# Kernel optimization log

Hardware: AMD Instinct MI355X
Metric: run time of the kernel (lower is better)

The kernel has to match this reference:

```python
import jax, jax.numpy as jnp
import numpy as np

B, N, H = 2, 1024, 768
MAX_W = 30
WIDTH_D = 20
SPAN_DIM = 3 * H + WIDTH_D  # 2324
K = int(N * 0.4)  # 409 (eval mode: // (1+0) )


def _enumerate_spans(n, max_w):
    # Replicates: enumerate_spans then sorted(spans[::-1], key=start)
    # -> start ascending, end DESCENDING within each start.
    spans = []
    for s in range(n):
        for e in range(min(s + max_w - 1, n - 1), s - 1, -1):
            spans.append((s, e))
    return np.asarray(spans, dtype=np.int32)  # [num_spans, 2]


def setup_inputs() -> dict:
    key = jax.random.key(0)
    ks = jax.random.split(key, 8)
    spans = jnp.asarray(_enumerate_spans(N, MAX_W))  # [30285, 2]
    return {
        "segment_embeddings": jax.random.normal(ks[0], (B, N, H), jnp.float32),
        "segment_mask": jnp.ones((B, N), jnp.int32),
        "candidate_spans": spans,
        "width_emb": jax.random.normal(ks[1], (MAX_W, WIDTH_D), jnp.float32) * 0.02,
        "W1": jax.random.normal(ks[2], (SPAN_DIM, H), jnp.float32) * 0.02,
        "b1": jax.random.normal(ks[3], (H,), jnp.float32) * 0.02,
        "w_s": jax.random.normal(ks[4], (H,), jnp.float32) * 0.02,
        "b_s": jax.random.normal(ks[5], (1,), jnp.float32) * 0.02,
        "k": K,
    }


def reference(segment_embeddings, segment_mask, candidate_spans, width_emb, W1, b1, w_s, b_s, k):
    starts = candidate_spans[:, 0]  # [S]
    ends = candidate_spans[:, 1]    # [S]
    # Endpoint span extractor: x, y, x*y + width embedding (width = end-start)
    x = segment_embeddings[:, starts, :]          # [B,S,H]
    y = segment_embeddings[:, ends, :]            # [B,S,H]
    wemb = width_emb[ends - starts]               # [S,WIDTH_D]
    bsz = segment_embeddings.shape[0]
    span_feat = jnp.concatenate(
        [x, y, x * y, jnp.broadcast_to(wemb[None], (bsz,) + wemb.shape)], axis=-1
    )  # [B,S,3H+WD]
    # MLP (dropout is identity in eval) + GELU (torch default: exact erf)
    h = jax.nn.gelu(jnp.einsum("bsd,dh->bsh", span_feat, W1) + b1, approximate=False)
    scores = jnp.einsum("bsh,h->bs", h, w_s) + b_s[0]  # [B,S]
    # Mask spans whose end index exceeds valid length
    lengths = segment_mask.sum(-1)  # [B]
    scores = scores + jnp.where(ends[None, :] >= lengths[:, None], -1e6, 0.0)
    # Top-k prune, then sort indices and gather
    _, idx = jax.lax.top_k(scores, k)          # [B,k]
    idx = jnp.sort(idx, axis=1)
    top_scores = jnp.take_along_axis(scores, idx, axis=1)            # [B,k]
    top_span_embs = jnp.take_along_axis(h, idx[:, :, None], axis=1)  # [B,k,H]
    top_spans = candidate_spans[idx]                                 # [B,k,2]
    return top_span_embs, top_scores, top_spans
```

## Files before the change

kernel.cpp:

```cpp
#include <hip/hip_runtime.h>
#include <math.h>

#define NB 2
#define NN 1024
#define HH 768
#define MAXW 30
#define KTOP 409
#define BANDCAP 4096
#define BAND_TAU 2e-2f
#define FILTCAP 6144
#define GROWS 512
#define WCAP 40

typedef __attribute__((ext_vector_type(4))) float f32x4;
typedef __attribute__((ext_vector_type(8))) __bf16 bf16x8;
typedef __attribute__((ext_vector_type(8))) unsigned short us8;

__device__ __forceinline__ float gelu_f(float z) {
  return 0.5f * z * (1.0f + erff(z * 0.70710678118654752440f));
}
__device__ __forceinline__ unsigned f2key(float f) {
  unsigned u = __float_as_uint(f);
  return (u & 0x80000000u) ? ~u : (u | 0x80000000u);
}
__device__ __forceinline__ float key2f(unsigned k) {
  unsigned u = (k & 0x80000000u) ? (k & 0x7fffffffu) : ~k;
  return __uint_as_float(u);
}
__device__ __forceinline__ unsigned short f2bf_rn(float f) {
  unsigned u = __float_as_uint(f);
  unsigned r = u + 0x7fffu + ((u >> 16) & 1u);
  return (unsigned short)(r >> 16);
}
__device__ __forceinline__ float bf2f(unsigned short h) {
  return __uint_as_float(((unsigned)h) << 16);
}
__device__ __forceinline__ void async_copy16(const void* g, void* l) {
  __builtin_amdgcn_global_load_lds(
      (const __attribute__((address_space(1))) unsigned int*)g,
      (__attribute__((address_space(3))) unsigned int*)l, 16, 0, 0);
}

__global__ void len_kernel(const int* __restrict__ mask, int* __restrict__ lengths) {
  __shared__ int red[256];
  for (int b = 0; b < NB; ++b) {
    int s = 0;
    for (int i = threadIdx.x; i < NN; i += 256) s += mask[b * NN + i];
    red[threadIdx.x] = s;
    __syncthreads();
    for (int off = 128; off > 0; off >>= 1) {
      if (threadIdx.x < off) red[threadIdx.x] += red[threadIdx.x + off];
      __syncthreads();
    }
    if (threadIdx.x == 0) lengths[b] = red[0];
    __syncthreads();
  }
}

__global__ void r_kernel(const float* __restrict__ wemb, const float* __restrict__ W1,
                         const float* __restrict__ b1, float* __restrict__ R) {
  int w = blockIdx.x;
  for (int h = threadIdx.x; h < HH; h += 256) {
    float acc = b1[h];
    for (int j = 0; j < 20; ++j)
      acc = fmaf(wemb[w * 20 + j], W1[(size_t)(3 * HH + j) * HH + h], acc);
    R[w * HH + h] = acc;
  }
}

__global__ __launch_bounds__(256) void prep_bt_kernel(const float* __restrict__ W1,
                                                      unsigned short* __restrict__ Bt,
                                                      unsigned short* __restrict__ Btlo) {
  const int ki = blockIdx.x;
  const int hby = blockIdx.y;
  const float* W1c = W1 + (size_t)(2 * HH) * HH;
  const int t = threadIdx.x;
#pragma unroll
  for (int half = 0; half < 2; ++half) {
    const int c = t + half * 256;
    const int col = c >> 2, kg = c & 3;
    us8 hv, lv;
#pragma unroll
    for (int j = 0; j < 8; ++j) {
      const int k = ki * 32 + kg * 8 + j;
      float v = W1c[(size_t)k * HH + hby * 128 + col];
      unsigned short h = f2bf_rn(v);
      hv[j] = h;
      lv[j] = f2bf_rn(v - bf2f(h));
    }
    const size_t bo = ((size_t)(hby * 24 + ki) * 512 + c) * 8;
    *(us8*)(Bt + bo) = hv;
    *(us8*)(Btlo + bo) = lv;
  }
}

__global__ __launch_bounds__(256) void prep_emb_hl_kernel(
    const float* __restrict__ emb, unsigned short* __restrict__ Ahi,
    unsigned short* __restrict__ Alo) {
  const int tile = blockIdx.x;
  const int ki = blockIdx.y;
  const int t = threadIdx.x;
#pragma unroll
  for (int half = 0; half < 2; ++half) {
    const int c = t + half * 256;
    const int row = c >> 2, kgs = c & 3;
    const int kg = kgs ^ ((row >> 1) & 3);
    const float* xr = emb + (size_t)(tile * 128 + row) * HH;
    const int k0 = ki * 32 + kg * 8;
    float4 x0 = *(const float4*)(xr + k0);
    float4 x1 = *(const float4*)(xr + k0 + 4);
    const float xv[8] = {x0.x, x0.y, x0.z, x0.w, x1.x, x1.y, x1.z, x1.w};
    us8 hv, lv;
#pragma unroll
    for (int j = 0; j < 8; ++j) {
      unsigned short h = f2bf_rn(xv[j]);
      hv[j] = h;
      lv[j] = f2bf_rn(xv[j] - bf2f(h));
    }
    const size_t base = (((size_t)tile * 24 + ki) * 512 + c) * 8;
    *(us8*)(Ahi + base) = hv;
    *(us8*)(Alo + base) = lv;
  }
}

__global__ __launch_bounds__(256) void prep_w1ab_kernel(
    const float* __restrict__ W1, unsigned short* __restrict__ Bhi,
    unsigned short* __restrict__ Blo) {
  const int ki = blockIdx.x;
  const int hby = blockIdx.y;
  const int t = threadIdx.x;
#pragma unroll
  for (int half = 0; half < 2; ++half) {
    const int c = t + half * 256;
    const int col = c >> 2, kg = c & 3;
    const int gc = hby * 128 + col;
    const float* base = W1 + (gc < 768 ? (size_t)0 : (size_t)HH * HH);
    const int n = (gc < 768) ? gc : gc - 768;
    us8 hv, lv;
#pragma unroll
    for (int j = 0; j < 8; ++j) {
      const int k = ki * 32 + kg * 8 + j;
      float v = base[(size_t)k * HH + n];
      unsigned short h = f2bf_rn(v);
      hv[j] = h;
      lv[j] = f2bf_rn(v - bf2f(h));
    }
    const size_t bo = (((size_t)hby * 24 + ki) * 512 + c) * 8;
    *(us8*)(Bhi + bo) = hv;
    *(us8*)(Blo + bo) = lv;
  }
}

__global__ __launch_bounds__(256) void pq_mfma_kernel(
    const unsigned short* __restrict__ Ahi, const unsigned short* __restrict__ Alo,
    const unsigned short* __restrict__ Bhi, const unsigned short* __restrict__ Blo,
    float* __restrict__ P, float* __restrict__ Q) {
  __shared__ unsigned short AsmH[128 * 32], AsmL[128 * 32];
  const int tile = blockIdx.x;
  const int hby = blockIdx.y;
  const int tid = threadIdx.x;
  const int lane = tid & 63, w = tid >> 6;
  const int wm = w & 1, wn = w >> 1;
  const int lm = lane & 15, lq = lane >> 4;

  f32x4 acc[4][4];
#pragma unroll
  for (int i = 0; i < 4; ++i)
#pragma unroll
    for (int j = 0; j < 4; ++j) acc[i][j] = (f32x4){0.f, 0.f, 0.f, 0.f};

  const unsigned short* AbH = Ahi + (size_t)tile * 24 * 4096;
  const unsigned short* AbL = Alo + (size_t)tile * 24 * 4096;
  const unsigned short* BbH = Bhi + (size_t)hby * 24 * 4096;
  const unsigned short* BbL = Blo + (size_t)hby * 24 * 4096;
  const int a_off = (wm * 64 + lm) * 32 + (lq ^ ((lm >> 1) & 3)) * 8;
  const int b_off = (wn * 64 + lm) * 32 + lq * 8;

  for (int ki = 0; ki < 24; ++ki) {
    async_copy16(AbH + (size_t)ki * 4096 + tid * 8, AsmH + tid * 8);
    async_copy16(AbH + (size_t)ki * 4096 + (tid + 256) * 8, AsmH + (tid + 256) * 8);
    async_copy16(AbL + (size_t)ki * 4096 + tid * 8, AsmL + tid * 8);
    async_copy16(AbL + (size_t)ki * 4096 + (tid + 256) * 8, AsmL + (tid + 256) * 8);
    bf16x8 bh[4], bl[4];
#pragma unroll
    for (int ni = 0; ni < 4; ++ni) {
      bh[ni] = *reinterpret_cast<const bf16x8*>(BbH + (size_t)ki * 4096 + b_off + ni * 512);
      bl[ni] = *reinterpret_cast<const bf16x8*>(BbL + (size_t)ki * 4096 + b_off + ni * 512);
    }
    __syncthreads();
    bf16x8 ah[4], al[4];
#pragma unroll
    for (int mi = 0; mi < 4; ++mi) {
      ah[mi] = *reinterpret_cast<const bf16x8*>(AsmH + a_off + mi * 512);
      al[mi] = *reinterpret_cast<const bf16x8*>(AsmL + a_off + mi * 512);
    }
#pragma unroll
    for (int ni = 0; ni < 4; ++ni)
#pragma unroll
      for (int mi = 0; mi < 4; ++mi) {
        acc[mi][ni] = __builtin_amdgcn_mfma_f32_16x16x32_bf16(ah[mi], bh[ni], acc[mi][ni], 0, 0, 0);
        acc[mi][ni] = __builtin_amdgcn_mfma_f32_16x16x32_bf16(ah[mi], bl[ni], acc[mi][ni], 0, 0, 0);
        acc[mi][ni] = __builtin_amdgcn_mfma_f32_16x16x32_bf16(al[mi], bh[ni], acc[mi][ni], 0, 0, 0);
      }
    __syncthreads();
  }

  float* Obase = (hby < 6) ? P : Q;
  const int cb = ((hby < 6) ? hby : hby - 6) * 128 + wn * 64 + lm;
  const int rowb = tile * 128 + wm * 64 + lq * 4;
#pragma unroll
  for (int mi = 0; mi < 4; ++mi)
#pragma unroll
    for (int ni = 0; ni < 4; ++ni)
#pragma unroll
      for (int r = 0; r < 4; ++r)
        Obase[(size_t)(rowb + mi * 16 + r) * HH + cb + ni * 16] = acc[mi][ni][r];
}

__global__ __launch_bounds__(512, 4) void score_mfma7_kernel(
    const float* __restrict__ emb, const int* __restrict__ spans,
    const unsigned short* __restrict__ Bt, const float* __restrict__ w_s,
    const float* __restrict__ P, const float* __restrict__ Q, const float* __restrict__ R,
    float* __restrict__ spart, int S) {
  __shared__ unsigned short Asm[128 * 32];
  __shared__ float ew[2][WCAP * 32];
  __shared__ int ssm[128], eem[128], wwm[128];
  __shared__ float sred[128 * 4];
  __shared__ int rminS, rmaxS;

  const int colblk = blockIdx.x;
  const int tile = blockIdx.y;
  const int b = blockIdx.z;
  const int tid = threadIdx.x;
  const int lane = tid & 63, w = tid >> 6;
  const int wm = w & 1, wn = w >> 1;
  const int lm = lane & 15, lq = lane >> 4;

  if (tid < 128) {
    int g = tile * 128 + tid;
    int gg = g < S ? g : S - 1;
    int s = spans[2 * gg], e = spans[2 * gg + 1];
    ssm[tid] = s; eem[tid] = e; wwm[tid] = e - s;
  }
  __syncthreads();
  if (tid == 0) {
    int rmn = ssm[0], rmx = eem[0];
    for (int i = 1; i < 128; ++i) {
      rmn = min(rmn, ssm[i]);
      rmx = max(rmx, eem[i]);
    }
    rminS = rmn; rmaxS = rmx;
  }
  __syncthreads();
  const int rmin = rminS;
  int W = rmaxS - rmin + 1;
  if (W > WCAP) W = WCAP;

  const int sr = tid >> 3, sc = (tid & 7) * 4;
  const bool stager = (tid < W * 8);
  const float* gsrc = emb + ((size_t)b * NN + rmin + sr) * HH + sc;
  const int ewoff = sr * 32 + sc;

  const int arow = tid >> 2;
  const int kgs = tid & 3;
  const int kg = kgs ^ ((arow >> 1) & 3);
  const int xo = (ssm[arow] - rmin) * 32 + kg * 8;
  const int yo = (eem[arow] - rmin) * 32 + kg * 8;
  const int aw_off = (arow * 4 + kgs) * 8;

  f32x4 acc[4][4];
#pragma unroll
  for (int i = 0; i < 4; ++i)
#pragma unroll
    for (int j = 0; j < 4; ++j) acc[i][j] = (f32x4){0.f, 0.f, 0.f, 0.f};

  const int hby = colblk * 2 + (wn >> 1);
  const unsigned short* Bb = Bt + (size_t)hby * 24 * 4096;
  const int b_off = ((wn & 1) * 64 + lm) * 32 + lq * 8;
  const int a_off = (wm * 64 + lm) * 32 + (lq ^ ((lm >> 1) & 3)) * 8;

  float4 reg = make_float4(0.f, 0.f, 0.f, 0.f);
  if (stager) {
    float4 r0 = *(const float4*)gsrc;
    *(float4*)(&ew[0][ewoff]) = r0;
    reg = *(const float4*)(gsrc + 32);
  }
  __syncthreads();

  int cur = 0;
  for (int ki = 0; ki < 24; ++ki) {
    float4 x0 = *(const float4*)(&ew[cur][xo]);
    float4 x1 = *(const float4*)(&ew[cur][xo + 4]);
    float4 y0 = *(const float4*)(&ew[cur][yo]);
    float4 y1 = *(const float4*)(&ew[cur][yo + 4]);
    us8 v;
    v[0] = f2bf_rn(x0.x * y0.x); v[1] = f2bf_rn(x0.y * y0.y);
    v[2] = f2bf_rn(x0.z * y0.z); v[3] = f2bf_rn(x0.w * y0.w);
    v[4] = f2bf_rn(x1.x * y1.x); v[5] = f2bf_rn(x1.y * y1.y);
    v[6] = f2bf_rn(x1.z * y1.z); v[7] = f2bf_rn(x1.w * y1.w);
    *(us8*)(Asm + aw_off) = v;
    if (stager && ki < 23) *(float4*)(&ew[1 - cur][ewoff]) = reg;
    __syncthreads();
    if (stager && ki + 2 < 24)
      reg = *(const float4*)(gsrc + (size_t)(ki + 2) * 32);
    bf16x8 afr[4];
#pragma unroll
    for (int mi = 0; mi < 4; ++mi)
      afr[mi] = *reinterpret_cast<const bf16x8*>(Asm + a_off + mi * 512);
#pragma unroll
    for (int ni = 0; ni < 4; ++ni) {
      bf16x8 bfr = *reinterpret_cast<const bf16x8*>(Bb + (size_t)ki * 4096 + b_off + ni * 512);
#pragma unroll
      for (int mi = 0; mi < 4; ++mi)
        acc[mi][ni] = __builtin_amdgcn_mfma_f32_16x16x32_bf16(afr[mi], bfr, acc[mi][ni], 0, 0, 0);
    }
    __syncthreads();
    cur ^= 1;
  }

  const int cbase = colblk * 256 + wn * 64 + lm;
  float wsv[4];
#pragma unroll
  for (int ni = 0; ni < 4; ++ni) wsv[ni] = w_s[cbase + ni * 16];

#pragma unroll
  for (int mi = 0; mi < 4; ++mi) {
#pragma unroll
    for (int r = 0; r < 4; ++r) {
      const int rowl = wm * 64 + mi * 16 + lq * 4 + r;
      const int s = ssm[rowl], e = eem[rowl], wd = wwm[rowl];
      const float* Pp = P + ((size_t)b * NN + s) * HH + cbase;
      const float* Qp = Q + ((size_t)b * NN + e) * HH + cbase;
      const float* Rp = R + (size_t)wd * HH + cbase;
      float psum = 0.f;
#pragma unroll
      for (int ni = 0; ni < 4; ++ni) {
        float z = acc[mi][ni][r] + Pp[ni * 16] + Qp[ni * 16] + Rp[ni * 16];
        psum = fmaf(gelu_f(z), wsv[ni], psum);
      }
      psum += __shfl_xor(psum, 1);
      psum += __shfl_xor(psum, 2);
      psum += __shfl_xor(psum, 4);
      psum += __shfl_xor(psum, 8);
      if (lm == 0) sred[rowl * 4 + wn] = psum;
    }
  }
  __syncthreads();
  if (tid < 128) {
    int g = tile * 128 + tid;
    if (g < S)
      spart[(size_t)colblk * ((size_t)NB * S) + (size_t)b * S + g] =
          sred[tid * 4] + sred[tid * 4 + 1] + sred[tid * 4 + 2] + sred[tid * 4 + 3];
  }
}

__global__ void combine_kernel(const float* __restrict__ sp, const int* __restrict__ spans,
                               const float* __restrict__ b_s, const int* __restrict__ lengths,
                               float* __restrict__ scores, int S) {
  int idx = blockIdx.x * 256 + threadIdx.x;
  if (idx >= NB * S) return;
  int b = idx / S, i = idx - b * S;
  size_t st = (size_t)NB * S;
  float v = b_s[0];
#pragma unroll
  for (int j = 0; j < 3; ++j) v += sp[j * st + idx];
  if (spans[2 * i + 1] >= lengths[b]) v += -1000000.0f;
  scores[idx] = v;
}

__global__ void zero_kernel(unsigned* __restrict__ hist, int* __restrict__ bandcount,
                            int* __restrict__ filtcount) {
  int i = blockIdx.x * 256 + threadIdx.x;
  hist[i] = 0;
  if (blockIdx.x == 0 && threadIdx.x < NB) {
    bandcount[threadIdx.x] = 0;
    filtcount[threadIdx.x] = 0;
  }
}

__global__ void hist16_kernel(const float* __restrict__ scores, unsigned* __restrict__ hist,
                              int S) {
  int idx = blockIdx.x * 256 + threadIdx.x;
  if (idx >= NB * S) return;
  int b = idx / S;
  unsigned key = f2key(scores[idx]) >> 16;
  atomicAdd(&hist[(size_t)b * 65536 + key], 1u);
}

__global__ __launch_bounds__(1024) void scan16_kernel(const unsigned* __restrict__ hist,
                                                      const int* __restrict__ kptr,
                                                      float* __restrict__ pivotf) {
  const int b = blockIdx.x;
  const unsigned* hb = hist + (size_t)b * 65536;
  const int tid = threadIdx.x;
  const unsigned k = (unsigned)kptr[0];
  __shared__ unsigned acc[1024];
  unsigned s = 0;
  for (int j = 0; j < 64; ++j) s += hb[tid * 64 + j];
  const unsigned mysum = s;
  acc[tid] = s;
  __syncthreads();
  for (int off = 1; off < 1024; off <<= 1) {
    unsigned v = (tid + off < 1024) ? acc[tid + off] : 0u;
    __syncthreads();
    acc[tid] += v;
    __syncthreads();
  }
  const unsigned above = acc[tid] - mysum;
  if (above < k && acc[tid] >= k) {
    unsigned cum = above;
    int binf = tid * 64;
    for (int j = 63; j >= 0; --j) {
      unsigned c = hb[tid * 64 + j];
      if (cum + c >= k) { binf = tid * 64 + j; break; }
      cum += c;
    }
    pivotf[b] = key2f(((unsigned)binf) << 16);
  }
}

__global__ void band_kernel(const float* __restrict__ scores, const float* __restrict__ pivotf,
                            int* __restrict__ bandcount, int* __restrict__ bandlist, int S) {
  int idx = blockIdx.x * 256 + threadIdx.x;
  if (idx >= NB * S) return;
  int b = idx / S, i = idx - b * S;
  if (fabsf(scores[idx] - pivotf[b]) <= BAND_TAU) {
    int slot = atomicAdd(&bandcount[b], 1);
    if (slot < BANDCAP) bandlist[b * BANDCAP + slot] = i;
  }
}

__global__ __launch_bounds__(256) void rescore_kernel(
    const float* __restrict__ emb, const int* __restrict__ spans,
    const float* __restrict__ W1, const float* __restrict__ w_s,
    const float* __restrict__ b_s, const int* __restrict__ lengths,
    const float* __restrict__ P, const float* __restrict__ Q, const float* __restrict__ R,
    const int* __restrict__ bandcount, const int* __restrict__ bandlist,
    float* __restrict__ scores, int S) {
  const int b = blockIdx.y;
  int cnt = bandcount[b];
  if (cnt > BANDCAP) cnt = BANDCAP;
  if ((int)blockIdx.x >= cnt) return;
  const int i = bandlist[b * BANDCAP + blockIdx.x];
  const int s = spans[2 * i], e = spans[2 * i + 1], wd = e - s;
  const int tid = threadIdx.x;
  __shared__ float prod[HH];
  __shared__ float red[256];
  for (int c = tid; c < HH; c += 256)
    prod[c] = emb[((size_t)b * NN + s) * HH + c] * emb[((size_t)b * NN + e) * HH + c];
  __syncthreads();
  const float* W1c = W1 + (size_t)(2 * HH) * HH;
  float psum = 0.f;
  for (int c0 = 0; c0 < HH; c0 += 256) {
    const int c = c0 + tid;
    float a = P[((size_t)b * NN + s) * HH + c] + Q[((size_t)b * NN + e) * HH + c] + R[(size_t)wd * HH + c];
    for (int k = 0; k < HH; ++k) a = fmaf(prod[k], W1c[(size_t)k * HH + c], a);
    psum = fmaf(gelu_f(a), w_s[c], psum);
  }
  red[tid] = psum;
  __syncthreads();
  for (int off = 128; off > 0; off >>= 1) {
    if (tid < off) red[tid] += red[tid + off];
    __syncthreads();
  }
  if (tid == 0) {
    float v = red[0] + b_s[0];
    if (e >= lengths[b]) v += -1000000.0f;
    scores[(size_t)b * S + i] = v;
  }
}

__global__ void filt_kernel(const float* __restrict__ scores, const float* __restrict__ pivotf,
                            int* __restrict__ filtcount, int* __restrict__ filtlist, int S) {
  int idx = blockIdx.x * 256 + threadIdx.x;
  if (idx >= NB * S) return;
  int b = idx / S, i = idx - b * S;
  if (scores[idx] > pivotf[b] - 0.01f) {
    int slot = atomicAdd(&filtcount[b], 1);
    if (slot < FILTCAP) filtlist[b * FILTCAP + slot] = i;
  }
}

__global__ __launch_bounds__(1024) void sel_kernel(
    const float* __restrict__ scores, const int* __restrict__ spans,
    const int* __restrict__ kptr, const int* __restrict__ filtcount,
    const int* __restrict__ filtlist,
    float* __restrict__ out_spans, int* __restrict__ sel, int S) {
  const int b = blockIdx.x;
  const int tid = threadIdx.x;
  const int k = kptr[0];
  __shared__ unsigned keys[FILTCAP];
  __shared__ int idxs[FILTCAP];
  __shared__ unsigned hist[256];
  __shared__ unsigned sh_prefix;
  __shared__ int sh_remaining;
  __shared__ int selcnt;
  __shared__ int slist[512];

  int M = filtcount[b];
  if (M > FILTCAP) M = FILTCAP;
  for (int i = tid; i < M; i += 1024) {
    int gi = filtlist[b * FILTCAP + i];
    idxs[i] = gi;
    keys[i] = f2key(scores[(size_t)b * S + gi]);
  }
  if (tid == 0) selcnt = 0;
  __syncthreads();

  unsigned prefix = 0;
  int remaining = k;
  for (int round = 0; round < 4; ++round) {
    const int shift = 24 - 8 * round;
    if (tid < 256) hist[tid] = 0;
    __syncthreads();
    for (int i = tid; i < M; i += 1024) {
      unsigned key = keys[i];
      if (round == 0 || (key >> (shift + 8)) == prefix)
        atomicAdd(&hist[(key >> shift) & 255u], 1u);
    }
    __syncthreads();
    if (tid == 0) {
      int cum = 0;
      for (int bin = 255; bin >= 0; --bin) {
        int c = (int)hist[bin];
        if (cum + c >= remaining) {
          sh_prefix = (prefix << 8) | (unsigned)bin;
          sh_remaining = remaining - cum;
          break;
        }
        cum += c;
      }
    }
    __syncthreads();
    prefix = sh_prefix;
    remaining = sh_remaining;
    __syncthreads();
  }
  const unsigned pk = prefix;
  const int m_eq = remaining;

  for (int i = tid; i < M; i += 1024) {
    unsigned key = keys[i];
    bool pick = false;
    if (key > pk) {
      pick = true;
    } else if (key == pk) {
      int r = 0;
      const int myidx = idxs[i];
      for (int j = 0; j < M; ++j)
        if (keys[j] == pk && idxs[j] < myidx) ++r;
      pick = (r < m_eq);
    }
    if (pick) {
      int p = atomicAdd(&selcnt, 1);
      if (p < 512) slist[p] = idxs[i];
    }
  }
  __syncthreads();

  for (int i = tid; i < k; i += 1024) {
    const int my = slist[i];
    int r = 0;
    for (int j = 0; j < k; ++j) r += (slist[j] < my);
    sel[b * KTOP + r] = my;
    out_spans[(b * KTOP + r) * 2 + 0] = (float)spans[2 * my];
    out_spans[(b * KTOP + r) * 2 + 1] = (float)spans[2 * my + 1];
  }
}

__global__ __launch_bounds__(256) void prep_ga_kernel(
    const float* __restrict__ emb, const int* __restrict__ spans,
    const int* __restrict__ sel, unsigned short* __restrict__ GAhi,
    unsigned short* __restrict__ GAlo) {
  const int bx = blockIdx.x;
  const int tile = bx / 24, ki = bx - tile * 24;
  const int b = blockIdx.y;
  const int t = threadIdx.x;
#pragma unroll
  for (int half = 0; half < 2; ++half) {
    const int c = t + half * 256;
    const int row = c >> 2, kgs = c & 3;
    const int kg = kgs ^ ((row >> 1) & 3);
    int j = tile * 128 + row;
    if (j >= KTOP) j = KTOP - 1;
    const int i = sel[b * KTOP + j];
    const int s = spans[2 * i], e = spans[2 * i + 1];
    const float* xr = emb + ((size_t)b * NN + s) * HH;
    const float* yr = emb + ((size_t)b * NN + e) * HH;
    const int k0 = ki * 32 + kg * 8;
    float4 x0 = *(const float4*)(xr + k0);
    float4 x1 = *(const float4*)(xr + k0 + 4);
    float4 y0 = *(const float4*)(yr + k0);
    float4 y1 = *(const float4*)(yr + k0 + 4);
    const float pv[8] = {x0.x * y0.x, x0.y * y0.y, x0.z * y0.z, x0.w * y0.w,
                         x1.x * y1.x, x1.y * y1.y, x1.z * y1.z, x1.w * y1.w};
    us8 hv, lv;
#pragma unroll
    for (int q = 0; q < 8; ++q) {
      unsigned short h = f2bf_rn(pv[q]);
      hv[q] = h;
      lv[q] = f2bf_rn(pv[q] - bf2f(h));
    }
    const size_t base = (((size_t)(b * 4 + tile) * 24 + ki) * 512 + c) * 8;
    *(us8*)(GAhi + base) = hv;
    *(us8*)(GAlo + base) = lv;
  }
}

__global__ __launch_bounds__(256) void gather_mfma_kernel(
    const int* __restrict__ spans, const int* __restrict__ sel,
    const unsigned short* __restrict__ GAhi, const unsigned short* __restrict__ GAlo,
    const unsigned short* __restrict__ Bt, const unsigned short* __restrict__ Btlo,
    const float* __restrict__ w_s,
    const float* __restrict__ P, const float* __restrict__ Q, const float* __restrict__ R,
    float* __restrict__ outh, float* __restrict__ spartg) {
  __shared__ unsigned short AsmH[128 * 32], AsmL[128 * 32];
  __shared__ int ssm[128], eem[128], wwm[128], vvm[128];
  __shared__ float sred[128 * 2];
  const int tile = blockIdx.x;
  const int hby = blockIdx.y;
  const int b = blockIdx.z;
  const int tid = threadIdx.x;
  const int lane = tid & 63, w = tid >> 6;
  const int wm = w & 1, wn = w >> 1;
  const int lm = lane & 15, lq = lane >> 4;

  if (tid < 128) {
    int j = tile * 128 + tid;
    int valid = (j < KTOP) ? 1 : 0;
    int jj = valid ? j : KTOP - 1;
    int i = sel[b * KTOP + jj];
    ssm[tid] = spans[2 * i];
    eem[tid] = spans[2 * i + 1];
    wwm[tid] = eem[tid] - ssm[tid];
    vvm[tid] = valid;
  }

  f32x4 acc[4][4];
#pragma unroll
  for (int i = 0; i < 4; ++i)
#pragma unroll
    for (int j = 0; j < 4; ++j) acc[i][j] = (f32x4){0.f, 0.f, 0.f, 0.f};

  const unsigned short* AbH = GAhi + (size_t)(b * 4 + tile) * 24 * 4096;
  const unsigned short* AbL = GAlo + (size_t)(b * 4 + tile) * 24 * 4096;
  const unsigned short* BbH = Bt + (size_t)hby * 24 * 4096;
  const unsigned short* BbL = Btlo + (size_t)hby * 24 * 4096;
  const int a_off = (wm * 64 + lm) * 32 + (lq ^ ((lm >> 1) & 3)) * 8;
  const int b_off = (wn * 64 + lm) * 32 + lq * 8;

  for (int ki = 0; ki < 24; ++ki) {
    async_copy16(AbH + (size_t)ki * 4096 + tid * 8, AsmH + tid * 8);
    async_copy16(AbH + (size_t)ki * 4096 + (tid + 256) * 8, AsmH + (tid + 256) * 8);
    async_copy16(AbL + (size_t)ki * 4096 + tid * 8, AsmL + tid * 8);
    async_copy16(AbL + (size_t)ki * 4096 + (tid + 256) * 8, AsmL + (tid + 256) * 8);
    bf16x8 bh[4], bl[4];
#pragma unroll
    for (int ni = 0; ni < 4; ++ni) {
      bh[ni] = *reinterpret_cast<const bf16x8*>(BbH + (size_t)ki * 4096 + b_off + ni * 512);
      bl[ni] = *reinterpret_cast<const bf16x8*>(BbL + (size_t)ki * 4096 + b_off + ni * 512);
    }
    __syncthreads();
    bf16x8 ah[4], al[4];
#pragma unroll
    for (int mi = 0; mi < 4; ++mi) {
      ah[mi] = *reinterpret_cast<const bf16x8*>(AsmH + a_off + mi * 512);
      al[mi] = *reinterpret_cast<const bf16x8*>(AsmL + a_off + mi * 512);
    }
#pragma unroll
    for (int ni = 0; ni < 4; ++ni)
#pragma unroll
      for (int mi = 0; mi < 4; ++mi) {
        acc[mi][ni] = __builtin_amdgcn_mfma_f32_16x16x32_bf16(ah[mi], bh[ni], acc[mi][ni], 0, 0, 0);
        acc[mi][ni] = __builtin_amdgcn_mfma_f32_16x16x32_bf16(ah[mi], bl[ni], acc[mi][ni], 0, 0, 0);
        acc[mi][ni] = __builtin_amdgcn_mfma_f32_16x16x32_bf16(al[mi], bh[ni], acc[mi][ni], 0, 0, 0);
      }
    __syncthreads();
  }

  const int hbg = hby * 128;
  float wsv[4];
#pragma unroll
  for (int ni = 0; ni < 4; ++ni) wsv[ni] = w_s[hbg + wn * 64 + ni * 16 + lm];

#pragma unroll
  for (int mi = 0; mi < 4; ++mi) {
#pragma unroll
    for (int r = 0; r < 4; ++r) {
      const int rowl = wm * 64 + mi * 16 + lq * 4 + r;
      const int s = ssm[rowl], e = eem[rowl], wd = wwm[rowl];
      const float* Pp = P + ((size_t)b * NN + s) * HH + hbg + wn * 64 + lm;
      const float* Qp = Q + ((size_t)b * NN + e) * HH + hbg + wn * 64 + lm;
      const float* Rp = R + (size_t)wd * HH + hbg + wn * 64 + lm;
      float psum = 0.f;
      const int j = tile * 128 + rowl;
      float* op = outh + (size_t)(b * KTOP + j) * HH + hbg + wn * 64 + lm;
#pragma unroll
      for (int ni = 0; ni < 4; ++ni) {
        float z = acc[mi][ni][r] + Pp[ni * 16] + Qp[ni * 16] + Rp[ni * 16];
        float gl = gelu_f(z);
        if (vvm[rowl]) op[ni * 16] = gl;
        psum = fmaf(gl, wsv[ni], psum);
      }
      psum += __shfl_xor(psum, 1);
      psum += __shfl_xor(psum, 2);
      psum += __shfl_xor(psum, 4);
      psum += __shfl_xor(psum, 8);
      if (lm == 0) sred[rowl * 2 + wn] = psum;
    }
  }
  __syncthreads();
  if (tid < 128)
    spartg[(size_t)hby * (NB * GROWS) + b * GROWS + tile * 128 + tid] =
        sred[tid * 2] + sred[tid * 2 + 1];
}

__global__ void score_fin_kernel(const float* __restrict__ spartg, const int* __restrict__ sel,
                                 const int* __restrict__ spans, const float* __restrict__ b_s,
                                 const int* __restrict__ lengths, float* __restrict__ out_scores) {
  int idx = blockIdx.x * 256 + threadIdx.x;
  if (idx >= NB * KTOP) return;
  int b = idx / KTOP, j = idx - b * KTOP;
  float v = b_s[0];
#pragma unroll
  for (int hby = 0; hby < 6; ++hby)
    v += spartg[(size_t)hby * (NB * GROWS) + b * GROWS + j];
  int i = sel[idx];
  if (spans[2 * i + 1] >= lengths[b]) v += -1000000.0f;
  out_scores[idx] = v;
}

extern "C" void kernel_launch(void* const* d_in, const int* in_sizes, int n_in,
                              void* d_out, int out_size, void* d_ws, size_t ws_size,
                              hipStream_t stream) {
  const float* emb = (const float*)d_in[0];
  const int* mask = (const int*)d_in[1];
  const int* spans = (const int*)d_in[2];
  const float* wemb = (const float*)d_in[3];
  const float* W1 = (const float*)d_in[4];
  const float* b1 = (const float*)d_in[5];
  const float* w_s = (const float*)d_in[6];
  const float* b_s = (const float*)d_in[7];
  const int* kptr = (const int*)d_in[8];
  const int S = in_sizes[2] / 2;
  float* out = (float*)d_out;

  char* wp = (char*)d_ws;
  auto take = [&](size_t bytes) {
    char* p = wp;
    wp += (bytes + 63) & ~(size_t)63;
    return p;
  };
  float* Pb = (float*)take((size_t)NB * NN * HH * 4);
  float* Qb = (float*)take((size_t)NB * NN * HH * 4);
  float* Rb = (float*)take((size_t)MAXW * HH * 4);
  float* spart = (float*)take(3 * (size_t)NB * S * 4);
  float* scoresb = (float*)take((size_t)NB * S * 4);
  float* spartg = (float*)take(6 * (size_t)NB * GROWS * 4);
  float* pivotf = (float*)take(NB * 4);
  unsigned short* AimgHi = (unsigned short*)take((size_t)16 * 24 * 4096 * 2);
  unsigned short* AimgLo = (unsigned short*)take((size_t)16 * 24 * 4096 * 2);
  unsigned short* BimgHi = (unsigned short*)take((size_t)12 * 24 * 4096 * 2);
  unsigned short* BimgLo = (unsigned short*)take((size_t)12 * 24 * 4096 * 2);
  unsigned short* Bt = (unsigned short*)take((size_t)6 * 24 * 4096 * 2);
  unsigned short* Btlo = (unsigned short*)take((size_t)6 * 24 * 4096 * 2);
  unsigned short* GAhi = (unsigned short*)take((size_t)NB * 4 * 24 * 4096 * 2);
  unsigned short* GAlo = (unsigned short*)take((size_t)NB * 4 * 24 * 4096 * 2);
  unsigned* hist16b = (unsigned*)take((size_t)NB * 65536 * 4);
  int* selb = (int*)take(NB * KTOP * 4);
  int* lengthsb = (int*)take(NB * 4);
  int* bandcount = (int*)take(NB * 4);
  int* bandlist = (int*)take((size_t)NB * BANDCAP * 4);
  int* filtcount = (int*)take(NB * 4);
  int* filtlist = (int*)take((size_t)NB * FILTCAP * 4);

  const size_t OFF1 = (size_t)NB * KTOP * HH;
  const size_t OFF2 = OFF1 + (size_t)NB * KTOP;

  const int tiles = (S + 127) / 128;

  len_kernel<<<dim3(1), dim3(256), 0, stream>>>(mask, lengthsb);
  r_kernel<<<dim3(MAXW), dim3(256), 0, stream>>>(wemb, W1, b1, Rb);
  prep_bt_kernel<<<dim3(24, 6), dim3(256), 0, stream>>>(W1, Bt, Btlo);
  prep_emb_hl_kernel<<<dim3(16, 24), dim3(256), 0, stream>>>(emb, AimgHi, AimgLo);
  prep_w1ab_kernel<<<dim3(24, 12), dim3(256), 0, stream>>>(W1, BimgHi, BimgLo);
  pq_mfma_kernel<<<dim3(16, 12), dim3(256), 0, stream>>>(AimgHi, AimgLo, BimgHi, BimgLo, Pb, Qb);
  zero_kernel<<<dim3(512), dim3(256), 0, stream>>>(hist16b, bandcount, filtcount);

  score_mfma7_kernel<<<dim3(3, tiles, NB), dim3(512), 0, stream>>>(
      emb, spans, Bt, w_s, Pb, Qb, Rb, spart, S);

  combine_kernel<<<dim3((NB * S + 255) / 256), dim3(256), 0, stream>>>(
      spart, spans, b_s, lengthsb, scoresb, S);
  hist16_kernel<<<dim3((NB * S + 255) / 256), dim3(256), 0, stream>>>(scoresb, hist16b, S);
  scan16_kernel<<<dim3(NB), dim3(1024), 0, stream>>>(hist16b, kptr, pivotf);
  band_kernel<<<dim3((NB * S + 255) / 256), dim3(256), 0, stream>>>(
      scoresb, pivotf, bandcount, bandlist, S);
  rescore_kernel<<<dim3(BANDCAP, NB), dim3(256), 0, stream>>>(
      emb, spans, W1, w_s, b_s, lengthsb, Pb, Qb, Rb, bandcount, bandlist, scoresb, S);
  filt_kernel<<<dim3((NB * S + 255) / 256), dim3(256), 0, stream>>>(
      scoresb, pivotf, filtcount, filtlist, S);
  sel_kernel<<<dim3(NB), dim3(1024), 0, stream>>>(
      scoresb, spans, kptr, filtcount, filtlist, out + OFF2, selb, S);
  prep_ga_kernel<<<dim3(96, NB), dim3(256), 0, stream>>>(emb, spans, selb, GAhi, GAlo);
  gather_mfma_kernel<<<dim3(4, 6, NB), dim3(256), 0, stream>>>(
      spans, selb, GAhi, GAlo, Bt, Btlo, w_s, Pb, Qb, Rb, out, spartg);
  score_fin_kernel<<<dim3((NB * KTOP + 255) / 256), dim3(256), 0, stream>>>(
      spartg, selb, spans, b_s, lengthsb, out + OFF1);
}
```

Measured before the change: 546.1 us.

## Fuse prep kernels, merge combine with histogram, software-pipeline score MFMA loop

Six small setup kernels (lengths, R table, weight and embedding bf16 split, histogram zeroing) become one launch that dispatches on block index. Score combination and histogram building now run in one kernel, which skips a re-read of the scores. The scoring MFMA kernel double-buffers its A tile in LDS and prefetches B fragments and staged embeddings one step ahead, so loads overlap the matrix math. The staging window now uses a fixed cap instead of the tile's span range. The larger LDS footprint lowers the occupancy hint from 4 to 3 blocks per CU.

```diff
diff --git a/kernel.cpp b/kernel.cpp
--- a/kernel.cpp
+++ b/kernel.cpp
@@ -41,113 +41,114 @@
       (__attribute__((address_space(3))) unsigned int*)l, 16, 0, 0);
 }
 
-__global__ void len_kernel(const int* __restrict__ mask, int* __restrict__ lengths) {
-  __shared__ int red[256];
-  for (int b = 0; b < NB; ++b) {
-    int s = 0;
-    for (int i = threadIdx.x; i < NN; i += 256) s += mask[b * NN + i];
-    red[threadIdx.x] = s;
-    __syncthreads();
-    for (int off = 128; off > 0; off >>= 1) {
-      if (threadIdx.x < off) red[threadIdx.x] += red[threadIdx.x + off];
+__global__ __launch_bounds__(256) void prep_all_kernel(
+    const int* __restrict__ mask, int* __restrict__ lengths,
+    const float* __restrict__ wemb, const float* __restrict__ W1,
+    const float* __restrict__ b1, float* __restrict__ R,
+    unsigned short* __restrict__ Bt, unsigned short* __restrict__ Btlo,
+    const float* __restrict__ emb,
+    unsigned short* __restrict__ Ahi, unsigned short* __restrict__ Alo,
+    unsigned short* __restrict__ Bhi, unsigned short* __restrict__ Blo,
+    unsigned* __restrict__ hist, int* __restrict__ bandcount, int* __restrict__ filtcount) {
+  const int bx = blockIdx.x;
+  const int t = threadIdx.x;
+  if (bx == 0) {
+    __shared__ int red[256];
+    for (int b = 0; b < NB; ++b) {
+      int s = 0;
+      for (int i = t; i < NN; i += 256) s += mask[b * NN + i];
+      red[t] = s;
       __syncthreads();
-    }
-    if (threadIdx.x == 0) lengths[b] = red[0];
-    __syncthreads();
-  }
-}
-
-__global__ void r_kernel(const float* __restrict__ wemb, const float* __restrict__ W1,
-                         const float* __restrict__ b1, float* __restrict__ R) {
-  int w = blockIdx.x;
-  for (int h = threadIdx.x; h < HH; h += 256) {
-    float acc = b1[h];
-    for (int j = 0; j < 20; ++j)
-      acc = fmaf(wemb[w * 20 + j], W1[(size_t)(3 * HH + j) * HH + h], acc);
-    R[w * HH + h] = acc;
-  }
-}
-
-__global__ __launch_bounds__(256) void prep_bt_kernel(const float* __restrict__ W1,
-                                                      unsigned short* __restrict__ Bt,
-                                                      unsigned short* __restrict__ Btlo) {
-  const int ki = blockIdx.x;
-  const int hby = blockIdx.y;
-  const float* W1c = W1 + (size_t)(2 * HH) * HH;
-  const int t = threadIdx.x;
-#pragma unroll
-  for (int half = 0; half < 2; ++half) {
-    const int c = t + half * 256;
-    const int col = c >> 2, kg = c & 3;
-    us8 hv, lv;
-#pragma unroll
-    for (int j = 0; j < 8; ++j) {
-      const int k = ki * 32 + kg * 8 + j;
-      float v = W1c[(size_t)k * HH + hby * 128 + col];
-      unsigned short h = f2bf_rn(v);
-      hv[j] = h;
-      lv[j] = f2bf_rn(v - bf2f(h));
-    }
-    const size_t bo = ((size_t)(hby * 24 + ki) * 512 + c) * 8;
-    *(us8*)(Bt + bo) = hv;
-    *(us8*)(Btlo + bo) = lv;
-  }
-}
-
-__global__ __launch_bounds__(256) void prep_emb_hl_kernel(
-    const float* __restrict__ emb, unsigned short* __restrict__ Ahi,
-    unsigned short* __restrict__ Alo) {
-  const int tile = blockIdx.x;
-  const int ki = blockIdx.y;
-  const int t = threadIdx.x;
-#pragma unroll
-  for (int half = 0; half < 2; ++half) {
-    const int c = t + half * 256;
-    const int row = c >> 2, kgs = c & 3;
-    const int kg = kgs ^ ((row >> 1) & 3);
-    const float* xr = emb + (size_t)(tile * 128 + row) * HH;
-    const int k0 = ki * 32 + kg * 8;
-    float4 x0 = *(const float4*)(xr + k0);
-    float4 x1 = *(const float4*)(xr + k0 + 4);
-    const float xv[8] = {x0.x, x0.y, x0.z, x0.w, x1.x, x1.y, x1.z, x1.w};
-    us8 hv, lv;
-#pragma unroll
-    for (int j = 0; j < 8; ++j) {
-      unsigned short h = f2bf_rn(xv[j]);
-      hv[j] = h;
-      lv[j] = f2bf_rn(xv[j] - bf2f(h));
-    }
-    const size_t base = (((size_t)tile * 24 + ki) * 512 + c) * 8;
-    *(us8*)(Ahi + base) = hv;
-    *(us8*)(Alo + base) = lv;
-  }
-}
-
-__global__ __launch_bounds__(256) void prep_w1ab_kernel(
-    const float* __restrict__ W1, unsigned short* __restrict__ Bhi,
-    unsigned short* __restrict__ Blo) {
-  const int ki = blockIdx.x;
-  const int hby = blockIdx.y;
-  const int t = threadIdx.x;
-#pragma unroll
-  for (int half = 0; half < 2; ++half) {
-    const int c = t + half * 256;
-    const int col = c >> 2, kg = c & 3;
-    const int gc = hby * 128 + col;
-    const float* base = W1 + (gc < 768 ? (size_t)0 : (size_t)HH * HH);
-    const int n = (gc < 768) ? gc : gc - 768;
-    us8 hv, lv;
-#pragma unroll
-    for (int j = 0; j < 8; ++j) {
-      const int k = ki * 32 + kg * 8 + j;
-      float v = base[(size_t)k * HH + n];
-      unsigned short h = f2bf_rn(v);
-      hv[j] = h;
-      lv[j] = f2bf_rn(v - bf2f(h));
-    }
-    const size_t bo = (((size_t)hby * 24 + ki) * 512 + c) * 8;
-    *(us8*)(Bhi + bo) = hv;
-    *(us8*)(Blo + bo) = lv;
+      for (int off = 128; off > 0; off >>= 1) {
+        if (t < off) red[t] += red[t + off];
+        __syncthreads();
+      }
+      if (t == 0) lengths[b] = red[0];
+      __syncthreads();
+    }
+  } else if (bx < 31) {
+    const int w = bx - 1;
+    for (int h = t; h < HH; h += 256) {
+      float acc = b1[h];
+      for (int j = 0; j < 20; ++j)
+        acc = fmaf(wemb[w * 20 + j], W1[(size_t)(3 * HH + j) * HH + h], acc);
+      R[w * HH + h] = acc;
+    }
+  } else if (bx < 175) {
+    const int l = bx - 31;
+    const int ki = l % 24, hby = l / 24;
+    const float* W1c = W1 + (size_t)(2 * HH) * HH;
+#pragma unroll
+    for (int half = 0; half < 2; ++half) {
+      const int c = t + half * 256;
+      const int col = c >> 2, kg = c & 3;
+      us8 hv, lv;
+#pragma unroll
+      for (int j = 0; j < 8; ++j) {
+        const int k = ki * 32 + kg * 8 + j;
+        float v = W1c[(size_t)k * HH + hby * 128 + col];
+        unsigned short h = f2bf_rn(v);
+        hv[j] = h;
+        lv[j] = f2bf_rn(v - bf2f(h));
+      }
+      const size_t bo = ((size_t)(hby * 24 + ki) * 512 + c) * 8;
+      *(us8*)(Bt + bo) = hv;
+      *(us8*)(Btlo + bo) = lv;
+    }
+  } else if (bx < 559) {
+    const int l = bx - 175;
+    const int tile = l / 24, ki = l % 24;
+#pragma unroll
+    for (int half = 0; half < 2; ++half) {
+      const int c = t + half * 256;
+      const int row = c >> 2, kgs = c & 3;
+      const int kg = kgs ^ ((row >> 1) & 3);
+      const float* xr = emb + (size_t)(tile * 128 + row) * HH;
+      const int k0 = ki * 32 + kg * 8;
+      float4 x0 = *(const float4*)(xr + k0);
+      float4 x1 = *(const float4*)(xr + k0 + 4);
+      const float xv[8] = {x0.x, x0.y, x0.z, x0.w, x1.x, x1.y, x1.z, x1.w};
+      us8 hv, lv;
+#pragma unroll
+      for (int j = 0; j < 8; ++j) {
+        unsigned short h = f2bf_rn(xv[j]);
+        hv[j] = h;
+        lv[j] = f2bf_rn(xv[j] - bf2f(h));
+      }
+      const size_t base = (((size_t)tile * 24 + ki) * 512 + c) * 8;
+      *(us8*)(Ahi + base) = hv;
+      *(us8*)(Alo + base) = lv;
+    }
+  } else if (bx < 847) {
+    const int l = bx - 559;
+    const int ki = l % 24, hby = l / 24;
+#pragma unroll
+    for (int half = 0; half < 2; ++half) {
+      const int c = t + half * 256;
+      const int col = c >> 2, kg = c & 3;
+      const int gc = hby * 128 + col;
+      const float* base = W1 + (gc < 768 ? (size_t)0 : (size_t)HH * HH);
+      const int n = (gc < 768) ? gc : gc - 768;
+      us8 hv, lv;
+#pragma unroll
+      for (int j = 0; j < 8; ++j) {
+        const int k = ki * 32 + kg * 8 + j;
+        float v = base[(size_t)k * HH + n];
+        unsigned short h = f2bf_rn(v);
+        hv[j] = h;
+        lv[j] = f2bf_rn(v - bf2f(h));
+      }
+      const size_t bo = (((size_t)hby * 24 + ki) * 512 + c) * 8;
+      *(us8*)(Bhi + bo) = hv;
+      *(us8*)(Blo + bo) = lv;
+    }
+  } else {
+    const int l = bx - 847;
+    hist[l * 256 + t] = 0;
+    if (l == 0 && t < NB) {
+      bandcount[t] = 0;
+      filtcount[t] = 0;
+    }
   }
 }
 
@@ -217,16 +218,16 @@
         Obase[(size_t)(rowb + mi * 16 + r) * HH + cb + ni * 16] = acc[mi][ni][r];
 }
 
-__global__ __launch_bounds__(512, 4) void score_mfma7_kernel(
+__global__ __launch_bounds__(512, 3) void score_mfma8_kernel(
     const float* __restrict__ emb, const int* __restrict__ spans,
     const unsigned short* __restrict__ Bt, const float* __restrict__ w_s,
     const float* __restrict__ P, const float* __restrict__ Q, const float* __restrict__ R,
     float* __restrict__ spart, int S) {
-  __shared__ unsigned short Asm[128 * 32];
+  __shared__ unsigned short Asm[2][128 * 32];
   __shared__ float ew[2][WCAP * 32];
   __shared__ int ssm[128], eem[128], wwm[128];
   __shared__ float sred[128 * 4];
-  __shared__ int rminS, rmaxS;
+  __shared__ int rminS;
 
   const int colblk = blockIdx.x;
   const int tile = blockIdx.y;
@@ -244,20 +245,16 @@
   }
   __syncthreads();
   if (tid == 0) {
-    int rmn = ssm[0], rmx = eem[0];
-    for (int i = 1; i < 128; ++i) {
-      rmn = min(rmn, ssm[i]);
-      rmx = max(rmx, eem[i]);
-    }
-    rminS = rmn; rmaxS = rmx;
+    int rmn = ssm[0];
+    for (int i = 1; i < 128; ++i) rmn = min(rmn, ssm[i]);
+    rminS = rmn;
   }
   __syncthreads();
   const int rmin = rminS;
-  int W = rmaxS - rmin + 1;
-  if (W > WCAP) W = WCAP;
 
   const int sr = tid >> 3, sc = (tid & 7) * 4;
-  const bool stager = (tid < W * 8);
+  const int wlim = min(WCAP, NN - rmin);
+  const bool stager = (tid < wlim * 8);
   const float* gsrc = emb + ((size_t)b * NN + rmin + sr) * HH + sc;
   const int ewoff = sr * 32 + sc;
 
@@ -279,40 +276,68 @@
   const int b_off = ((wn & 1) * 64 + lm) * 32 + lq * 8;
   const int a_off = (wm * 64 + lm) * 32 + (lq ^ ((lm >> 1) & 3)) * 8;
 
-  float4 reg = make_float4(0.f, 0.f, 0.f, 0.f);
   if (stager) {
     float4 r0 = *(const float4*)gsrc;
+    float4 r1 = *(const float4*)(gsrc + 32);
     *(float4*)(&ew[0][ewoff]) = r0;
-    reg = *(const float4*)(gsrc + 32);
-  }
-  __syncthreads();
-
-  int cur = 0;
-  for (int ki = 0; ki < 24; ++ki) {
-    float4 x0 = *(const float4*)(&ew[cur][xo]);
-    float4 x1 = *(const float4*)(&ew[cur][xo + 4]);
-    float4 y0 = *(const float4*)(&ew[cur][yo]);
-    float4 y1 = *(const float4*)(&ew[cur][yo + 4]);
+    *(float4*)(&ew[1][ewoff]) = r1;
+  }
+  __syncthreads();
+  {
+    float4 x0 = *(const float4*)(&ew[0][xo]);
+    float4 x1 = *(const float4*)(&ew[0][xo + 4]);
+    float4 y0 = *(const float4*)(&ew[0][yo]);
+    float4 y1 = *(const float4*)(&ew[0][yo + 4]);
     us8 v;
     v[0] = f2bf_rn(x0.x * y0.x); v[1] = f2bf_rn(x0.y * y0.y);
     v[2] = f2bf_rn(x0.z * y0.z); v[3] = f2bf_rn(x0.w * y0.w);
     v[4] = f2bf_rn(x1.x * y1.x); v[5] = f2bf_rn(x1.y * y1.y);
     v[6] = f2bf_rn(x1.z * y1.z); v[7] = f2bf_rn(x1.w * y1.w);
-    *(us8*)(Asm + aw_off) = v;
-    if (stager && ki < 23) *(float4*)(&ew[1 - cur][ewoff]) = reg;
-    __syncthreads();
-    if (stager && ki + 2 < 24)
-      reg = *(const float4*)(gsrc + (size_t)(ki + 2) * 32);
+    *(us8*)(&Asm[0][aw_off]) = v;
+  }
+  bf16x8 breg[4];
+#pragma unroll
+  for (int ni = 0; ni < 4; ++ni)
+    breg[ni] = *reinterpret_cast<const bf16x8*>(Bb + b_off + ni * 512);
+  float4 reg = make_float4(0.f, 0.f, 0.f, 0.f);
+  if (stager) reg = *(const float4*)(gsrc + 2 * 32);
+  __syncthreads();
+
+  int cur = 0;
+  for (int ki = 0; ki < 24; ++ki) {
     bf16x8 afr[4];
 #pragma unroll
     for (int mi = 0; mi < 4; ++mi)
-      afr[mi] = *reinterpret_cast<const bf16x8*>(Asm + a_off + mi * 512);
-#pragma unroll
-    for (int ni = 0; ni < 4; ++ni) {
-      bf16x8 bfr = *reinterpret_cast<const bf16x8*>(Bb + (size_t)ki * 4096 + b_off + ni * 512);
+      afr[mi] = *reinterpret_cast<const bf16x8*>(&Asm[cur][a_off + mi * 512]);
+    bf16x8 bnext[4];
+    if (ki < 23) {
+#pragma unroll
+      for (int ni = 0; ni < 4; ++ni)
+        bnext[ni] = *reinterpret_cast<const bf16x8*>(Bb + (size_t)(ki + 1) * 4096 + b_off + ni * 512);
+    }
+    if (ki < 23) {
+      const float* e1 = ew[(ki + 1) & 1];
+      float4 x0 = *(const float4*)(&e1[xo]);
+      float4 x1 = *(const float4*)(&e1[xo + 4]);
+      float4 y0 = *(const float4*)(&e1[yo]);
+      float4 y1 = *(const float4*)(&e1[yo + 4]);
+      us8 v;
+      v[0] = f2bf_rn(x0.x * y0.x); v[1] = f2bf_rn(x0.y * y0.y);
+      v[2] = f2bf_rn(x0.z * y0.z); v[3] = f2bf_rn(x0.w * y0.w);
+      v[4] = f2bf_rn(x1.x * y1.x); v[5] = f2bf_rn(x1.y * y1.y);
+      v[6] = f2bf_rn(x1.z * y1.z); v[7] = f2bf_rn(x1.w * y1.w);
+      *(us8*)(&Asm[cur ^ 1][aw_off]) = v;
+    }
+    if (stager && ki + 2 < 24) *(float4*)(&ew[ki & 1][ewoff]) = reg;
+    if (stager && ki + 3 < 24) reg = *(const float4*)(gsrc + (size_t)(ki + 3) * 32);
+#pragma unroll
+    for (int ni = 0; ni < 4; ++ni)
 #pragma unroll
       for (int mi = 0; mi < 4; ++mi)
-        acc[mi][ni] = __builtin_amdgcn_mfma_f32_16x16x32_bf16(afr[mi], bfr, acc[mi][ni], 0, 0, 0);
+        acc[mi][ni] = __builtin_amdgcn_mfma_f32_16x16x32_bf16(afr[mi], breg[ni], acc[mi][ni], 0, 0, 0);
+    if (ki < 23) {
+#pragma unroll
+      for (int ni = 0; ni < 4; ++ni) breg[ni] = bnext[ni];
     }
     __syncthreads();
     cur ^= 1;
@@ -354,9 +379,10 @@
   }
 }
 
-__global__ void combine_kernel(const float* __restrict__ sp, const int* __restrict__ spans,
-                               const float* __restrict__ b_s, const int* __restrict__ lengths,
-                               float* __restrict__ scores, int S) {
+__global__ void combine_hist_kernel(const float* __restrict__ sp, const int* __restrict__ spans,
+                                    const float* __restrict__ b_s, const int* __restrict__ lengths,
+                                    float* __restrict__ scores, unsigned* __restrict__ hist,
+                                    int S) {
   int idx = blockIdx.x * 256 + threadIdx.x;
   if (idx >= NB * S) return;
   int b = idx / S, i = idx - b * S;
@@ -366,24 +392,7 @@
   for (int j = 0; j < 3; ++j) v += sp[j * st + idx];
   if (spans[2 * i + 1] >= lengths[b]) v += -1000000.0f;
   scores[idx] = v;
-}
-
-__global__ void zero_kernel(unsigned* __restrict__ hist, int* __restrict__ bandcount,
-                            int* __restrict__ filtcount) {
-  int i = blockIdx.x * 256 + threadIdx.x;
-  hist[i] = 0;
-  if (blockIdx.x == 0 && threadIdx.x < NB) {
-    bandcount[threadIdx.x] = 0;
-    filtcount[threadIdx.x] = 0;
-  }
-}
-
-__global__ void hist16_kernel(const float* __restrict__ scores, unsigned* __restrict__ hist,
-                              int S) {
-  int idx = blockIdx.x * 256 + threadIdx.x;
-  if (idx >= NB * S) return;
-  int b = idx / S;
-  unsigned key = f2key(scores[idx]) >> 16;
+  unsigned key = f2key(v) >> 16;
   atomicAdd(&hist[(size_t)b * 65536 + key], 1u);
 }
 
@@ -779,20 +788,14 @@
 
   const int tiles = (S + 127) / 128;
 
-  len_kernel<<<dim3(1), dim3(256), 0, stream>>>(mask, lengthsb);
-  r_kernel<<<dim3(MAXW), dim3(256), 0, stream>>>(wemb, W1, b1, Rb);
-  prep_bt_kernel<<<dim3(24, 6), dim3(256), 0, stream>>>(W1, Bt, Btlo);
-  prep_emb_hl_kernel<<<dim3(16, 24), dim3(256), 0, stream>>>(emb, AimgHi, AimgLo);
-  prep_w1ab_kernel<<<dim3(24, 12), dim3(256), 0, stream>>>(W1, BimgHi, BimgLo);
+  prep_all_kernel<<<dim3(1359), dim3(256), 0, stream>>>(
+      mask, lengthsb, wemb, W1, b1, Rb, Bt, Btlo, emb, AimgHi, AimgLo, BimgHi, BimgLo,
+      hist16b, bandcount, filtcount);
   pq_mfma_kernel<<<dim3(16, 12), dim3(256), 0, stream>>>(AimgHi, AimgLo, BimgHi, BimgLo, Pb, Qb);
-  zero_kernel<<<dim3(512), dim3(256), 0, stream>>>(hist16b, bandcount, filtcount);
-
-  score_mfma7_kernel<<<dim3(3, tiles, NB), dim3(512), 0, stream>>>(
+  score_mfma8_kernel<<<dim3(3, tiles, NB), dim3(512), 0, stream>>>(
       emb, spans, Bt, w_s, Pb, Qb, Rb, spart, S);
-
-  combine_kernel<<<dim3((NB * S + 255) / 256), dim3(256), 0, stream>>>(
-      spart, spans, b_s, lengthsb, scoresb, S);
-  hist16_kernel<<<dim3((NB * S + 255) / 256), dim3(256), 0, stream>>>(scoresb, hist16b, S);
+  combine_hist_kernel<<<dim3((NB * S + 255) / 256), dim3(256), 0, stream>>>(
+      spart, spans, b_s, lengthsb, scoresb, hist16b, S);
   scan16_kernel<<<dim3(NB), dim3(1024), 0, stream>>>(hist16b, kptr, pivotf);
   band_kernel<<<dim3((NB * S + 255) / 256), dim3(256), 0, stream>>>(
       scoresb, pivotf, bandcount, bandlist, S);
```

Result: slower. 571.9 us (+4.7%).
